# Kernel optimization log

Hardware: AMD Instinct MI355X
Metric: run time of the kernel (lower is better)

Reference implementation:

```python
import jax, jax.numpy as jnp
import numpy as np

NUM_INPUTS = 1024
NUM_HIDDEN = 1024
FORGET_GATE_BIAS = -1.0
EPS = 1e-5


def layer_norm_1d(x, weight, bias):
    # Matches torch LayerNorm1D: std is unbiased (ddof=1), divide by (std + eps)
    mean = jnp.mean(x, axis=1, keepdims=True)
    std = jnp.std(x, axis=1, keepdims=True, ddof=1)
    return (x - mean) / (std + EPS) * weight + bias


def setup_inputs() -> dict:
    key = jax.random.key(0)
    ks = jax.random.split(key, 8)
    B, I, H = 4096, NUM_INPUTS, NUM_HIDDEN
    lim_i = 1.0 / np.sqrt(I)
    lim_h = 1.0 / np.sqrt(H)
    return {
        "inputs": jax.random.normal(ks[0], (B, I), jnp.float32),
        "hx": jax.random.normal(ks[1], (B, H), jnp.float32),
        "cx": jax.random.normal(ks[2], (B, H), jnp.float32),
        "w_i2h": jax.random.uniform(ks[3], (4 * H, I), jnp.float32, -lim_i, lim_i),
        "b_i2h": jax.random.uniform(ks[4], (4 * H,), jnp.float32, -lim_i, lim_i),
        "w_h2h": jax.random.uniform(ks[5], (4 * H, H), jnp.float32, -lim_h, lim_h),
        "b_h2h": jax.random.uniform(ks[6], (4 * H,), jnp.float32, -lim_h, lim_h),
        "ln_i2h_w": jnp.ones((1, 4 * H), jnp.float32),
        "ln_i2h_b": jnp.zeros((1, 4 * H), jnp.float32),
        "ln_h2h_w": jnp.ones((1, 4 * H), jnp.float32),
        "ln_h2h_b": jnp.zeros((1, 4 * H), jnp.float32),
        "ln_h2o_w": jnp.ones((1, H), jnp.float32),
        "ln_h2o_b": jnp.zeros((1, H), jnp.float32),
    }


def reference(inputs, hx, cx, w_i2h, b_i2h, w_h2h, b_h2h,
              ln_i2h_w, ln_i2h_b, ln_h2h_w, ln_h2h_b, ln_h2o_w, ln_h2o_b):
    H = NUM_HIDDEN
    i2h = inputs @ w_i2h.T + b_i2h          # [B, 4H]
    h2h = hx @ w_h2h.T + b_h2h              # [B, 4H]
    x = layer_norm_1d(i2h, ln_i2h_w, ln_i2h_b) + layer_norm_1d(h2h, ln_h2h_w, ln_h2h_b)
    g_i, g_f, g_o, g_c = jnp.split(x, 4, axis=1)
    in_gate = jax.nn.sigmoid(g_i)
    forget_gate = jax.nn.sigmoid(g_f + FORGET_GATE_BIAS)
    out_gate = jax.nn.sigmoid(g_o)
    in_transform = jnp.tanh(g_c)
    cx_new = forget_gate * cx + in_gate * in_transform
    hx_new = out_gate * jnp.tanh(layer_norm_1d(cx_new, ln_h2o_w, ln_h2o_b))
    return hx_new, cx_new
```

## Files before the change

### kernel.cpp

```cpp
#include <hip/hip_runtime.h>
#include <hip/hip_bf16.h>
#include <math.h>

#define NI 1024
#define NH 1024
#define H4 4096
#define FGB (-1.0f)
#define LN_EPS 1e-5f
#define NKT 32

typedef unsigned short u16;
typedef __attribute__((ext_vector_type(8))) short short8;
typedef __attribute__((ext_vector_type(8))) unsigned short ushort8v;
typedef __attribute__((ext_vector_type(16))) float f32x16;

__device__ __forceinline__ float bf2f(u16 u) {
    union { unsigned int i; float f; } v; v.i = ((unsigned int)u) << 16; return v.f;
}
__device__ __forceinline__ u16 f2bf(float f) {
    __hip_bfloat16 h = __float2bfloat16(f);
    return __builtin_bit_cast(u16, h);
}
__device__ __forceinline__ float fast_sigmoid(float x) {
    return 1.0f / (1.0f + __expf(-x));
}
__device__ __forceinline__ float fast_tanh(float x) {
    return 1.0f - 2.0f / (__expf(2.0f * x) + 1.0f);
}

__device__ __forceinline__ void gload16(const u16* g, u16* l) {
    __builtin_amdgcn_global_load_lds(
        (const __attribute__((address_space(1))) void*)g,
        (__attribute__((address_space(3))) void*)l,
        16, 0, 0);
}

__global__ __launch_bounds__(256) void shuffle_cast(
    const float* __restrict__ a, const float* __restrict__ b,
    const float* __restrict__ c, const float* __restrict__ d,
    u16* __restrict__ oa, u16* __restrict__ ob,
    u16* __restrict__ oc, u16* __restrict__ od)
{
    __shared__ u16 sT[32][264];

    const int my = blockIdx.y;
    const float* src = (my == 0) ? a : (my == 1) ? b : (my == 2) ? c : d;
    u16*         dst = (my == 0) ? oa : (my == 1) ? ob : (my == 2) ? oc : od;

    const int mtile = blockIdx.x >> 2;
    const int slab  = blockIdx.x & 3;
    const int t     = threadIdx.x;
    const int w     = t >> 6;
    const int lane  = t & 63;

    const float* s0 = src + (size_t)(mtile * 32) * 1024 + slab * 256 + lane * 4;
#pragma unroll
    for (int i = 0; i < 8; ++i) {
        const int row = i * 4 + w;
        float4 v = *(const float4*)(s0 + (size_t)row * 1024);
        ushort4 pk;
        pk.x = f2bf(v.x); pk.y = f2bf(v.y); pk.z = f2bf(v.z); pk.w = f2bf(v.w);
        *(ushort4*)&sT[row][lane * 4] = pk;
    }
    __syncthreads();

    const int r  = lane & 31;
    const int hi = lane >> 5;
#pragma unroll
    for (int j = 0; j < 2; ++j) {
        const int ktl = w * 2 + j;
        const int kt  = slab * 8 + ktl;
        u16* o = dst + ((size_t)(mtile * 32 + kt)) * 1024 + lane * 8;
#pragma unroll
        for (int kh = 0; kh < 2; ++kh) {
            ushort8v vv = *(const ushort8v*)&sT[r][ktl * 32 + kh * 16 + hi * 8];
            *(ushort8v*)(o + kh * 512) = vv;
        }
    }
}

__global__ __launch_bounds__(512, 2) void gemm_lds(
    const u16* __restrict__ Af0, const u16* __restrict__ Wf0,
    const float* __restrict__ bias0, u16* __restrict__ C0,
    const u16* __restrict__ Af1, const u16* __restrict__ Wf1,
    const float* __restrict__ bias1, u16* __restrict__ C1,
    int N)
{
    const u16*   Af   = blockIdx.z ? Af1 : Af0;
    const u16*   Wf   = blockIdx.z ? Wf1 : Wf0;
    const float* bias = blockIdx.z ? bias1 : bias0;
    u16*         C    = blockIdx.z ? C1 : C0;

    __shared__ __align__(16) u16 sA[4][8][2][512];
    __shared__ __align__(16) u16 sB[4][8][2][512];

    const int tid  = threadIdx.x;
    const int lane = tid & 63;
    const int wave = tid >> 6;
    const int wm   = wave >> 2;
    const int wn   = wave & 3;

    const u16* gA = Af + (size_t)(blockIdx.y * 8 + wave) * 32768 + lane * 8;
    const u16* gB = Wf + (size_t)(blockIdx.x * 8 + wave) * 32768 + lane * 8;

    f32x16 acc[4][2];
#pragma unroll
    for (int i = 0; i < 4; ++i)
#pragma unroll
        for (int j = 0; j < 2; ++j)
#pragma unroll
            for (int r = 0; r < 16; ++r)
                acc[i][j][r] = 0.f;

#define STAGE(kt)                                                            \
    do {                                                                     \
        gload16(gA + (size_t)(kt) * 1024,       &sA[(kt) & 3][wave][0][0]);  \
        gload16(gA + (size_t)(kt) * 1024 + 512, &sA[(kt) & 3][wave][1][0]);  \
        gload16(gB + (size_t)(kt) * 1024,       &sB[(kt) & 3][wave][0][0]);  \
        gload16(gB + (size_t)(kt) * 1024 + 512, &sB[(kt) & 3][wave][1][0]);  \
    } while (0)

    ushort8v a0_0, a1_0, a2_0, a3_0, b0_0, b1_0;
    ushort8v a0_1, a1_1, a2_1, a3_1, b0_1, b1_1;

#define R0(slot)                                                             \
    do {                                                                     \
        a0_0 = *(const ushort8v*)&sA[slot][wm * 4 + 0][0][lane * 8];         \
        a1_0 = *(const ushort8v*)&sA[slot][wm * 4 + 1][0][lane * 8];         \
        b0_0 = *(const ushort8v*)&sB[slot][wn * 2 + 0][0][lane * 8];         \
        b1_0 = *(const ushort8v*)&sB[slot][wn * 2 + 1][0][lane * 8];         \
        a2_0 = *(const ushort8v*)&sA[slot][wm * 4 + 2][0][lane * 8];         \
        a3_0 = *(const ushort8v*)&sA[slot][wm * 4 + 3][0][lane * 8];         \
    } while (0)
#define R1(slot)                                                             \
    do {                                                                     \
        a0_1 = *(const ushort8v*)&sA[slot][wm * 4 + 0][1][lane * 8];         \
        a1_1 = *(const ushort8v*)&sA[slot][wm * 4 + 1][1][lane * 8];         \
        b0_1 = *(const ushort8v*)&sB[slot][wn * 2 + 0][1][lane * 8];         \
        b1_1 = *(const ushort8v*)&sB[slot][wn * 2 + 1][1][lane * 8];         \
        a2_1 = *(const ushort8v*)&sA[slot][wm * 4 + 2][1][lane * 8];         \
        a3_1 = *(const ushort8v*)&sA[slot][wm * 4 + 3][1][lane * 8];         \
    } while (0)

#define M8(aa0, aa1, aa2, aa3, bb0, bb1)                                                             \
    do {                                                                                             \
        __builtin_amdgcn_s_setprio(1);                                                               \
        acc[0][0] = __builtin_amdgcn_mfma_f32_32x32x16_bf16((short8)aa0, (short8)bb0, acc[0][0], 0, 0, 0); \
        acc[1][0] = __builtin_amdgcn_mfma_f32_32x32x16_bf16((short8)aa1, (short8)bb0, acc[1][0], 0, 0, 0); \
        acc[0][1] = __builtin_amdgcn_mfma_f32_32x32x16_bf16((short8)aa0, (short8)bb1, acc[0][1], 0, 0, 0); \
        acc[1][1] = __builtin_amdgcn_mfma_f32_32x32x16_bf16((short8)aa1, (short8)bb1, acc[1][1], 0, 0, 0); \
        acc[2][0] = __builtin_amdgcn_mfma_f32_32x32x16_bf16((short8)aa2, (short8)bb0, acc[2][0], 0, 0, 0); \
        acc[3][0] = __builtin_amdgcn_mfma_f32_32x32x16_bf16((short8)aa3, (short8)bb0, acc[3][0], 0, 0, 0); \
        acc[2][1] = __builtin_amdgcn_mfma_f32_32x32x16_bf16((short8)aa2, (short8)bb1, acc[2][1], 0, 0, 0); \
        acc[3][1] = __builtin_amdgcn_mfma_f32_32x32x16_bf16((short8)aa3, (short8)bb1, acc[3][1], 0, 0, 0); \
        __builtin_amdgcn_s_setprio(0);                                                               \
    } while (0)

#define M8_SET0() M8(a0_0, a1_0, a2_0, a3_0, b0_0, b1_0)
#define M8_SET1() M8(a0_1, a1_1, a2_1, a3_1, b0_1, b1_1)

#define FENCE() asm volatile("" ::: "memory")

    STAGE(0);
    STAGE(1);
    asm volatile("s_waitcnt vmcnt(4)" ::: "memory");
    FENCE();
    __builtin_amdgcn_s_barrier();
    FENCE();
    STAGE(2);
    R0(0);
    R1(0);
    M8_SET0();

#pragma unroll
    for (int kt = 1; kt < NKT; ++kt) {
        const int slot = kt & 3;
        if (kt == NKT - 1) {
            asm volatile("s_waitcnt vmcnt(0)" ::: "memory");
        } else {
            asm volatile("s_waitcnt vmcnt(4)" ::: "memory");
        }
        FENCE();
        __builtin_amdgcn_s_barrier();
        FENCE();
        if (kt + 2 < NKT) STAGE(kt + 2);
        R0(slot);
        M8_SET1();
        R1(slot);
        M8_SET0();
    }
    M8_SET1();

#undef STAGE
#undef R0
#undef R1
#undef M8
#undef M8_SET0
#undef M8_SET1
#undef FENCE

    const int m0  = blockIdx.y * 256;
    const int n0  = blockIdx.x * 256;
    const int l31 = lane & 31;
    float bv[2];
#pragma unroll
    for (int tn = 0; tn < 2; ++tn)
        bv[tn] = bias[n0 + wn * 64 + tn * 32 + l31];

    const int rbase = (lane >> 5) * 4;
#pragma unroll
    for (int tm = 0; tm < 4; ++tm)
#pragma unroll
        for (int reg = 0; reg < 16; ++reg) {
            const int row = m0 + wm * 128 + tm * 32 + (reg & 3) + 8 * (reg >> 2) + rbase;
#pragma unroll
            for (int tn = 0; tn < 2; ++tn) {
                const int col = n0 + wn * 64 + tn * 32 + l31;
                C[(size_t)row * N + col] = f2bf(acc[tm][tn][reg] + bv[tn]);
            }
        }
}

__global__ __launch_bounds__(256) void lstm_pointwise(
    const u16* __restrict__ i2h, const u16* __restrict__ h2h,
    const float* __restrict__ cx,
    const float* __restrict__ lwx, const float* __restrict__ lbx,
    const float* __restrict__ lwy, const float* __restrict__ lby,
    const float* __restrict__ lwc, const float* __restrict__ lbc,
    float* __restrict__ hx_out, float* __restrict__ cx_out)
{
    __shared__ u16 sX[H4];
    __shared__ u16 sY[H4];
    __shared__ float red[16];

    const int row  = blockIdx.x;
    const int tid  = threadIdx.x;
    const int lane = tid & 63;
    const int wid  = tid >> 6;

    const u16* xr = i2h + (size_t)row * H4;
    const u16* yr = h2h + (size_t)row * H4;

    float sx = 0.f, sxx = 0.f, sy = 0.f, syy = 0.f;
#pragma unroll
    for (int s = 0; s < 2; ++s) {
        const int off = s * 2048 + tid * 8;
        ushort8v xv = *(const ushort8v*)(xr + off);
        ushort8v yv = *(const ushort8v*)(yr + off);
        *(ushort8v*)(sX + off) = xv;
        *(ushort8v*)(sY + off) = yv;
#pragma unroll
        for (int e = 0; e < 8; ++e) {
            float x = bf2f(xv[e]), y = bf2f(yv[e]);
            sx += x; sxx += x * x; sy += y; syy += y * y;
        }
    }
#pragma unroll
    for (int m = 32; m; m >>= 1) {
        sx  += __shfl_xor(sx,  m, 64);
        sxx += __shfl_xor(sxx, m, 64);
        sy  += __shfl_xor(sy,  m, 64);
        syy += __shfl_xor(syy, m, 64);
    }
    if (lane == 0) {
        red[wid] = sx; red[4 + wid] = sxx; red[8 + wid] = sy; red[12 + wid] = syy;
    }
    __syncthreads();
    const float tsx  = red[0] + red[1] + red[2] + red[3];
    const float tsxx = red[4] + red[5] + red[6] + red[7];
    const float tsy  = red[8] + red[9] + red[10] + red[11];
    const float tsyy = red[12] + red[13] + red[14] + red[15];
    __syncthreads();

    const float n1  = (float)H4;
    const float mx  = tsx / n1;
    const float ivx = 1.0f / (sqrtf(fmaxf((tsxx - tsx * tsx / n1) / (n1 - 1.f), 0.f)) + LN_EPS);
    const float my  = tsy / n1;
    const float ivy = 1.0f / (sqrtf(fmaxf((tsyy - tsy * tsy / n1) / (n1 - 1.f), 0.f)) + LN_EPS);

    const int j0 = tid * 4;
    float gate[4][4];
#pragma unroll
    for (int g = 0; g < 4; ++g) {
        ushort4 xv = *(const ushort4*)(sX + g * NH + j0);
        ushort4 yv = *(const ushort4*)(sY + g * NH + j0);
        float4 wxv = *(const float4*)(lwx + g * NH + j0);
        float4 bxv = *(const float4*)(lbx + g * NH + j0);
        float4 wyv = *(const float4*)(lwy + g * NH + j0);
        float4 byv = *(const float4*)(lby + g * NH + j0);
        gate[g][0] = (bf2f(xv.x) - mx) * ivx * wxv.x + bxv.x + (bf2f(yv.x) - my) * ivy * wyv.x + byv.x;
        gate[g][1] = (bf2f(xv.y) - mx) * ivx * wxv.y + bxv.y + (bf2f(yv.y) - my) * ivy * wyv.y + byv.y;
        gate[g][2] = (bf2f(xv.z) - mx) * ivx * wxv.z + bxv.z + (bf2f(yv.z) - my) * ivy * wyv.z + byv.z;
        gate[g][3] = (bf2f(xv.w) - mx) * ivx * wxv.w + bxv.w + (bf2f(yv.w) - my) * ivy * wyv.w + byv.w;
    }

    float4 cxv = *(const float4*)(cx + (size_t)row * NH + j0);
    const float cin[4] = {cxv.x, cxv.y, cxv.z, cxv.w};
    float cvl[4], og[4];
    float sc = 0.f, scc = 0.f;
#pragma unroll
    for (int e = 0; e < 4; ++e) {
        float ing = fast_sigmoid(gate[0][e]);
        float fg  = fast_sigmoid(gate[1][e] + FGB);
        og[e]     = fast_sigmoid(gate[2][e]);
        float tr  = fast_tanh(gate[3][e]);
        float c   = fg * cin[e] + ing * tr;
        cvl[e] = c; sc += c; scc += c * c;
    }
    *(float4*)(cx_out + (size_t)row * NH + j0) = make_float4(cvl[0], cvl[1], cvl[2], cvl[3]);

#pragma unroll
    for (int m = 32; m; m >>= 1) {
        sc  += __shfl_xor(sc,  m, 64);
        scc += __shfl_xor(scc, m, 64);
    }
    if (lane == 0) { red[wid] = sc; red[4 + wid] = scc; }
    __syncthreads();
    const float tsc  = red[0] + red[1] + red[2] + red[3];
    const float tscc = red[4] + red[5] + red[6] + red[7];

    const float nc  = (float)NH;
    const float mc  = tsc / nc;
    const float ivc = 1.0f / (sqrtf(fmaxf((tscc - tsc * tsc / nc) / (nc - 1.f), 0.f)) + LN_EPS);

    float4 wcv = *(const float4*)(lwc + j0);
    float4 bcv = *(const float4*)(lbc + j0);
    float h0 = og[0] * fast_tanh((cvl[0] - mc) * ivc * wcv.x + bcv.x);
    float h1 = og[1] * fast_tanh((cvl[1] - mc) * ivc * wcv.y + bcv.y);
    float h2 = og[2] * fast_tanh((cvl[2] - mc) * ivc * wcv.z + bcv.z);
    float h3 = og[3] * fast_tanh((cvl[3] - mc) * ivc * wcv.w + bcv.w);
    *(float4*)(hx_out + (size_t)row * NH + j0) = make_float4(h0, h1, h2, h3);
}

extern "C" void kernel_launch(void* const* d_in, const int* in_sizes, int n_in,
                              void* d_out, int out_size, void* d_ws, size_t ws_size,
                              hipStream_t stream) {
    const float* inputs = (const float*)d_in[0];
    const float* hx     = (const float*)d_in[1];
    const float* cx     = (const float*)d_in[2];
    const float* w_i2h  = (const float*)d_in[3];
    const float* b_i2h  = (const float*)d_in[4];
    const float* w_h2h  = (const float*)d_in[5];
    const float* b_h2h  = (const float*)d_in[6];
    const float* lwx    = (const float*)d_in[7];
    const float* lbx    = (const float*)d_in[8];
    const float* lwy    = (const float*)d_in[9];
    const float* lby    = (const float*)d_in[10];
    const float* lwc    = (const float*)d_in[11];
    const float* lbc    = (const float*)d_in[12];

    const int B = in_sizes[0] / NI;

    u16* a_fr   = (u16*)d_ws;
    u16* hx_fr  = a_fr   + (size_t)B * NI;
    u16* wi_fr  = hx_fr  + (size_t)B * NH;
    u16* wh_fr  = wi_fr  + (size_t)H4 * NI;
    u16* i2h_bf = wh_fr  + (size_t)H4 * NH;
    u16* h2h_bf = i2h_bf + (size_t)B * H4;

    float* hx_out = (float*)d_out;
    float* cx_out = hx_out + (size_t)B * NH;

    shuffle_cast<<<dim3(512, 4), dim3(256), 0, stream>>>(
        inputs, hx, w_i2h, w_h2h, a_fr, hx_fr, wi_fr, wh_fr);

    gemm_lds<<<dim3(H4 / 256, B / 256, 2), dim3(512), 0, stream>>>(
        a_fr, wi_fr, b_i2h, i2h_bf,
        hx_fr, wh_fr, b_h2h, h2h_bf,
        H4);

    lstm_pointwise<<<dim3(B), dim3(256), 0, stream>>>(
        i2h_bf, h2h_bf, cx, lwx, lbx, lwy, lby, lwc, lbc, hx_out, cx_out);
}
```

Baseline: 245.0 us.

## Use 4 waves per GEMM block with 128x128 warp tiles

Measured after the change: 250.7 us. +2.3%, slower.

```diff
diff --git a/kernel.cpp b/kernel.cpp
--- a/kernel.cpp
+++ b/kernel.cpp
@@ -79,7 +79,7 @@
     }
 }
 
-__global__ __launch_bounds__(512, 2) void gemm_lds(
+__global__ __launch_bounds__(256, 1) void gemm_lds(
     const u16* __restrict__ Af0, const u16* __restrict__ Wf0,
     const float* __restrict__ bias0, u16* __restrict__ C0,
     const u16* __restrict__ Af1, const u16* __restrict__ Wf1,
@@ -97,80 +97,90 @@
     const int tid  = threadIdx.x;
     const int lane = tid & 63;
     const int wave = tid >> 6;
-    const int wm   = wave >> 2;
-    const int wn   = wave & 3;
-
-    const u16* gA = Af + (size_t)(blockIdx.y * 8 + wave) * 32768 + lane * 8;
-    const u16* gB = Wf + (size_t)(blockIdx.x * 8 + wave) * 32768 + lane * 8;
-
-    f32x16 acc[4][2];
+    const int wm   = wave >> 1;
+    const int wn   = wave & 1;
+
+    const u16* gA0 = Af + (size_t)(blockIdx.y * 8 + wave * 2 + 0) * 32768 + lane * 8;
+    const u16* gA1 = Af + (size_t)(blockIdx.y * 8 + wave * 2 + 1) * 32768 + lane * 8;
+    const u16* gB0 = Wf + (size_t)(blockIdx.x * 8 + wave * 2 + 0) * 32768 + lane * 8;
+    const u16* gB1 = Wf + (size_t)(blockIdx.x * 8 + wave * 2 + 1) * 32768 + lane * 8;
+
+    f32x16 acc[4][4];
 #pragma unroll
     for (int i = 0; i < 4; ++i)
 #pragma unroll
-        for (int j = 0; j < 2; ++j)
+        for (int j = 0; j < 4; ++j)
 #pragma unroll
             for (int r = 0; r < 16; ++r)
                 acc[i][j][r] = 0.f;
 
-#define STAGE(kt)                                                            \
-    do {                                                                     \
-        gload16(gA + (size_t)(kt) * 1024,       &sA[(kt) & 3][wave][0][0]);  \
-        gload16(gA + (size_t)(kt) * 1024 + 512, &sA[(kt) & 3][wave][1][0]);  \
-        gload16(gB + (size_t)(kt) * 1024,       &sB[(kt) & 3][wave][0][0]);  \
-        gload16(gB + (size_t)(kt) * 1024 + 512, &sB[(kt) & 3][wave][1][0]);  \
+#define STAGE(kt)                                                             \
+    do {                                                                      \
+        gload16(gA0 + (size_t)(kt) * 1024,       &sA[(kt) & 3][wave * 2 + 0][0][0]); \
+        gload16(gA0 + (size_t)(kt) * 1024 + 512, &sA[(kt) & 3][wave * 2 + 0][1][0]); \
+        gload16(gA1 + (size_t)(kt) * 1024,       &sA[(kt) & 3][wave * 2 + 1][0][0]); \
+        gload16(gA1 + (size_t)(kt) * 1024 + 512, &sA[(kt) & 3][wave * 2 + 1][1][0]); \
+        gload16(gB0 + (size_t)(kt) * 1024,       &sB[(kt) & 3][wave * 2 + 0][0][0]); \
+        gload16(gB0 + (size_t)(kt) * 1024 + 512, &sB[(kt) & 3][wave * 2 + 0][1][0]); \
+        gload16(gB1 + (size_t)(kt) * 1024,       &sB[(kt) & 3][wave * 2 + 1][0][0]); \
+        gload16(gB1 + (size_t)(kt) * 1024 + 512, &sB[(kt) & 3][wave * 2 + 1][1][0]); \
     } while (0)
 
-    ushort8v a0_0, a1_0, a2_0, a3_0, b0_0, b1_0;
-    ushort8v a0_1, a1_1, a2_1, a3_1, b0_1, b1_1;
+    ushort8v a0_0, a1_0, a2_0, a3_0, b0_0, b1_0, b2_0, b3_0;
+    ushort8v a0_1, a1_1, a2_1, a3_1, b0_1, b1_1, b2_1, b3_1;
 
 #define R0(slot)                                                             \
     do {                                                                     \
         a0_0 = *(const ushort8v*)&sA[slot][wm * 4 + 0][0][lane * 8];         \
+        b0_0 = *(const ushort8v*)&sB[slot][wn * 4 + 0][0][lane * 8];         \
         a1_0 = *(const ushort8v*)&sA[slot][wm * 4 + 1][0][lane * 8];         \
-        b0_0 = *(const ushort8v*)&sB[slot][wn * 2 + 0][0][lane * 8];         \
-        b1_0 = *(const ushort8v*)&sB[slot][wn * 2 + 1][0][lane * 8];         \
+        b1_0 = *(const ushort8v*)&sB[slot][wn * 4 + 1][0][lane * 8];         \
         a2_0 = *(const ushort8v*)&sA[slot][wm * 4 + 2][0][lane * 8];         \
+        b2_0 = *(const ushort8v*)&sB[slot][wn * 4 + 2][0][lane * 8];         \
         a3_0 = *(const ushort8v*)&sA[slot][wm * 4 + 3][0][lane * 8];         \
+        b3_0 = *(const ushort8v*)&sB[slot][wn * 4 + 3][0][lane * 8];         \
     } while (0)
 #define R1(slot)                                                             \
     do {                                                                     \
         a0_1 = *(const ushort8v*)&sA[slot][wm * 4 + 0][1][lane * 8];         \
+        b0_1 = *(const ushort8v*)&sB[slot][wn * 4 + 0][1][lane * 8];         \
         a1_1 = *(const ushort8v*)&sA[slot][wm * 4 + 1][1][lane * 8];         \
-        b0_1 = *(const ushort8v*)&sB[slot][wn * 2 + 0][1][lane * 8];         \
-        b1_1 = *(const ushort8v*)&sB[slot][wn * 2 + 1][1][lane * 8];         \
+        b1_1 = *(const ushort8v*)&sB[slot][wn * 4 + 1][1][lane * 8];         \
         a2_1 = *(const ushort8v*)&sA[slot][wm * 4 + 2][1][lane * 8];         \
+        b2_1 = *(const ushort8v*)&sB[slot][wn * 4 + 2][1][lane * 8];         \
         a3_1 = *(const ushort8v*)&sA[slot][wm * 4 + 3][1][lane * 8];         \
+        b3_1 = *(const ushort8v*)&sB[slot][wn * 4 + 3][1][lane * 8];         \
     } while (0)
 
-#define M8(aa0, aa1, aa2, aa3, bb0, bb1)                                                             \
-    do {                                                                                             \
-        __builtin_amdgcn_s_setprio(1);                                                               \
-        acc[0][0] = __builtin_amdgcn_mfma_f32_32x32x16_bf16((short8)aa0, (short8)bb0, acc[0][0], 0, 0, 0); \
-        acc[1][0] = __builtin_amdgcn_mfma_f32_32x32x16_bf16((short8)aa1, (short8)bb0, acc[1][0], 0, 0, 0); \
-        acc[0][1] = __builtin_amdgcn_mfma_f32_32x32x16_bf16((short8)aa0, (short8)bb1, acc[0][1], 0, 0, 0); \
-        acc[1][1] = __builtin_amdgcn_mfma_f32_32x32x16_bf16((short8)aa1, (short8)bb1, acc[1][1], 0, 0, 0); \
-        acc[2][0] = __builtin_amdgcn_mfma_f32_32x32x16_bf16((short8)aa2, (short8)bb0, acc[2][0], 0, 0, 0); \
-        acc[3][0] = __builtin_amdgcn_mfma_f32_32x32x16_bf16((short8)aa3, (short8)bb0, acc[3][0], 0, 0, 0); \
-        acc[2][1] = __builtin_amdgcn_mfma_f32_32x32x16_bf16((short8)aa2, (short8)bb1, acc[2][1], 0, 0, 0); \
-        acc[3][1] = __builtin_amdgcn_mfma_f32_32x32x16_bf16((short8)aa3, (short8)bb1, acc[3][1], 0, 0, 0); \
-        __builtin_amdgcn_s_setprio(0);                                                               \
+#define MM(i, j, aa, bb) \
+    acc[i][j] = __builtin_amdgcn_mfma_f32_32x32x16_bf16((short8)aa, (short8)bb, acc[i][j], 0, 0, 0)
+
+#define M16(s)                                                               \
+    do {                                                                     \
+        __builtin_amdgcn_s_setprio(1);                                       \
+        MM(0, 0, a0_##s, b0_##s); MM(1, 0, a1_##s, b0_##s);                  \
+        MM(0, 1, a0_##s, b1_##s); MM(1, 1, a1_##s, b1_##s);                  \
+        MM(2, 0, a2_##s, b0_##s); MM(3, 0, a3_##s, b0_##s);                  \
+        MM(2, 1, a2_##s, b1_##s); MM(3, 1, a3_##s, b1_##s);                  \
+        MM(0, 2, a0_##s, b2_##s); MM(1, 2, a1_##s, b2_##s);                  \
+        MM(0, 3, a0_##s, b3_##s); MM(1, 3, a1_##s, b3_##s);                  \
+        MM(2, 2, a2_##s, b2_##s); MM(3, 2, a3_##s, b2_##s);                  \
+        MM(2, 3, a2_##s, b3_##s); MM(3, 3, a3_##s, b3_##s);                  \
+        __builtin_amdgcn_s_setprio(0);                                       \
     } while (0)
-
-#define M8_SET0() M8(a0_0, a1_0, a2_0, a3_0, b0_0, b1_0)
-#define M8_SET1() M8(a0_1, a1_1, a2_1, a3_1, b0_1, b1_1)
 
 #define FENCE() asm volatile("" ::: "memory")
 
     STAGE(0);
     STAGE(1);
-    asm volatile("s_waitcnt vmcnt(4)" ::: "memory");
+    asm volatile("s_waitcnt vmcnt(8)" ::: "memory");
     FENCE();
     __builtin_amdgcn_s_barrier();
     FENCE();
     STAGE(2);
     R0(0);
     R1(0);
-    M8_SET0();
+    M16(0);
 
 #pragma unroll
     for (int kt = 1; kt < NKT; ++kt) {
@@ -178,34 +188,33 @@
         if (kt == NKT - 1) {
             asm volatile("s_waitcnt vmcnt(0)" ::: "memory");
         } else {
-            asm volatile("s_waitcnt vmcnt(4)" ::: "memory");
+            asm volatile("s_waitcnt vmcnt(8)" ::: "memory");
         }
         FENCE();
         __builtin_amdgcn_s_barrier();
         FENCE();
         if (kt + 2 < NKT) STAGE(kt + 2);
         R0(slot);
-        M8_SET1();
+        M16(1);
         R1(slot);
-        M8_SET0();
-    }
-    M8_SET1();
+        M16(0);
+    }
+    M16(1);
 
 #undef STAGE
 #undef R0
 #undef R1
-#undef M8
-#undef M8_SET0
-#undef M8_SET1
+#undef MM
+#undef M16
 #undef FENCE
 
     const int m0  = blockIdx.y * 256;
     const int n0  = blockIdx.x * 256;
     const int l31 = lane & 31;
-    float bv[2];
-#pragma unroll
-    for (int tn = 0; tn < 2; ++tn)
-        bv[tn] = bias[n0 + wn * 64 + tn * 32 + l31];
+    float bv[4];
+#pragma unroll
+    for (int tn = 0; tn < 4; ++tn)
+        bv[tn] = bias[n0 + wn * 128 + tn * 32 + l31];
 
     const int rbase = (lane >> 5) * 4;
 #pragma unroll
@@ -214,8 +223,8 @@
         for (int reg = 0; reg < 16; ++reg) {
             const int row = m0 + wm * 128 + tm * 32 + (reg & 3) + 8 * (reg >> 2) + rbase;
 #pragma unroll
-            for (int tn = 0; tn < 2; ++tn) {
-                const int col = n0 + wn * 64 + tn * 32 + l31;
+            for (int tn = 0; tn < 4; ++tn) {
+                const int col = n0 + wn * 128 + tn * 32 + l31;
                 C[(size_t)row * N + col] = f2bf(acc[tm][tn][reg] + bv[tn]);
             }
         }
@@ -364,7 +373,7 @@
     shuffle_cast<<<dim3(512, 4), dim3(256), 0, stream>>>(
         inputs, hx, w_i2h, w_h2h, a_fr, hx_fr, wi_fr, wh_fr);
 
-    gemm_lds<<<dim3(H4 / 256, B / 256, 2), dim3(512), 0, stream>>>(
+    gemm_lds<<<dim3(H4 / 256, B / 256, 2), dim3(256), 0, stream>>>(
         a_fr, wi_fr, b_i2h, i2h_bf,
         hx_fr, wh_fr, b_h2h, h2h_bf,
         H4);
```

## Stagger LDS reads and MFMA order across wave pairs; keep pointwise rows in registers

Applied to the files above, without the earlier changes.

Result: faster. 237.6 us (-3.0%).

```diff
diff --git a/kernel.cpp b/kernel.cpp
--- a/kernel.cpp
+++ b/kernel.cpp
@@ -126,8 +126,8 @@
 #define R0(slot)                                                             \
     do {                                                                     \
         a0_0 = *(const ushort8v*)&sA[slot][wm * 4 + 0][0][lane * 8];         \
+        b0_0 = *(const ushort8v*)&sB[slot][wn * 2 + 0][0][lane * 8];         \
         a1_0 = *(const ushort8v*)&sA[slot][wm * 4 + 1][0][lane * 8];         \
-        b0_0 = *(const ushort8v*)&sB[slot][wn * 2 + 0][0][lane * 8];         \
         b1_0 = *(const ushort8v*)&sB[slot][wn * 2 + 1][0][lane * 8];         \
         a2_0 = *(const ushort8v*)&sA[slot][wm * 4 + 2][0][lane * 8];         \
         a3_0 = *(const ushort8v*)&sA[slot][wm * 4 + 3][0][lane * 8];         \
@@ -135,31 +135,39 @@
 #define R1(slot)                                                             \
     do {                                                                     \
         a0_1 = *(const ushort8v*)&sA[slot][wm * 4 + 0][1][lane * 8];         \
+        b0_1 = *(const ushort8v*)&sB[slot][wn * 2 + 0][1][lane * 8];         \
         a1_1 = *(const ushort8v*)&sA[slot][wm * 4 + 1][1][lane * 8];         \
-        b0_1 = *(const ushort8v*)&sB[slot][wn * 2 + 0][1][lane * 8];         \
         b1_1 = *(const ushort8v*)&sB[slot][wn * 2 + 1][1][lane * 8];         \
         a2_1 = *(const ushort8v*)&sA[slot][wm * 4 + 2][1][lane * 8];         \
         a3_1 = *(const ushort8v*)&sA[slot][wm * 4 + 3][1][lane * 8];         \
     } while (0)
 
-#define M8(aa0, aa1, aa2, aa3, bb0, bb1)                                                             \
-    do {                                                                                             \
-        __builtin_amdgcn_s_setprio(1);                                                               \
-        acc[0][0] = __builtin_amdgcn_mfma_f32_32x32x16_bf16((short8)aa0, (short8)bb0, acc[0][0], 0, 0, 0); \
-        acc[1][0] = __builtin_amdgcn_mfma_f32_32x32x16_bf16((short8)aa1, (short8)bb0, acc[1][0], 0, 0, 0); \
-        acc[0][1] = __builtin_amdgcn_mfma_f32_32x32x16_bf16((short8)aa0, (short8)bb1, acc[0][1], 0, 0, 0); \
-        acc[1][1] = __builtin_amdgcn_mfma_f32_32x32x16_bf16((short8)aa1, (short8)bb1, acc[1][1], 0, 0, 0); \
-        acc[2][0] = __builtin_amdgcn_mfma_f32_32x32x16_bf16((short8)aa2, (short8)bb0, acc[2][0], 0, 0, 0); \
-        acc[3][0] = __builtin_amdgcn_mfma_f32_32x32x16_bf16((short8)aa3, (short8)bb0, acc[3][0], 0, 0, 0); \
-        acc[2][1] = __builtin_amdgcn_mfma_f32_32x32x16_bf16((short8)aa2, (short8)bb1, acc[2][1], 0, 0, 0); \
-        acc[3][1] = __builtin_amdgcn_mfma_f32_32x32x16_bf16((short8)aa3, (short8)bb1, acc[3][1], 0, 0, 0); \
-        __builtin_amdgcn_s_setprio(0);                                                               \
-    } while (0)
-
-#define M8_SET0() M8(a0_0, a1_0, a2_0, a3_0, b0_0, b1_0)
-#define M8_SET1() M8(a0_1, a1_1, a2_1, a3_1, b0_1, b1_1)
+#define MM(i, j, aa, bb) \
+    acc[i][j] = __builtin_amdgcn_mfma_f32_32x32x16_bf16((short8)aa, (short8)bb, acc[i][j], 0, 0, 0)
+
+#define M8(s)                                                                \
+    do {                                                                     \
+        __builtin_amdgcn_s_setprio(1);                                       \
+        MM(0, 0, a0_##s, b0_##s); MM(1, 0, a1_##s, b0_##s);                  \
+        MM(0, 1, a0_##s, b1_##s); MM(1, 1, a1_##s, b1_##s);                  \
+        MM(2, 0, a2_##s, b0_##s); MM(3, 0, a3_##s, b0_##s);                  \
+        MM(2, 1, a2_##s, b1_##s); MM(3, 1, a3_##s, b1_##s);                  \
+        __builtin_amdgcn_s_setprio(0);                                       \
+    } while (0)
 
 #define FENCE() asm volatile("" ::: "memory")
+#define WIN_TOP(kt)                                                          \
+    do {                                                                     \
+        if ((kt) == NKT - 1) {                                               \
+            asm volatile("s_waitcnt vmcnt(0)" ::: "memory");                 \
+        } else {                                                             \
+            asm volatile("s_waitcnt vmcnt(4)" ::: "memory");                 \
+        }                                                                    \
+        FENCE();                                                             \
+        __builtin_amdgcn_s_barrier();                                        \
+        FENCE();                                                             \
+        if ((kt) + 2 < NKT) STAGE((kt) + 2);                                 \
+    } while (0)
 
     STAGE(0);
     STAGE(1);
@@ -170,33 +178,38 @@
     STAGE(2);
     R0(0);
     R1(0);
-    M8_SET0();
-
-#pragma unroll
-    for (int kt = 1; kt < NKT; ++kt) {
-        const int slot = kt & 3;
-        if (kt == NKT - 1) {
-            asm volatile("s_waitcnt vmcnt(0)" ::: "memory");
-        } else {
-            asm volatile("s_waitcnt vmcnt(4)" ::: "memory");
-        }
-        FENCE();
-        __builtin_amdgcn_s_barrier();
-        FENCE();
-        if (kt + 2 < NKT) STAGE(kt + 2);
-        R0(slot);
-        M8_SET1();
-        R1(slot);
-        M8_SET0();
-    }
-    M8_SET1();
+    M8(0);
+
+    if ((wave & 1) == 0) {
+#pragma unroll
+        for (int kt = 1; kt < NKT; ++kt) {
+            const int slot = kt & 3;
+            WIN_TOP(kt);
+            R0(slot);
+            M8(1);
+            R1(slot);
+            M8(0);
+        }
+    } else {
+#pragma unroll
+        for (int kt = 1; kt < NKT; ++kt) {
+            const int slot = kt & 3;
+            WIN_TOP(kt);
+            M8(1);
+            __builtin_amdgcn_sched_barrier(0);
+            R0(slot);
+            R1(slot);
+            M8(0);
+        }
+    }
+    M8(1);
 
 #undef STAGE
 #undef R0
 #undef R1
+#undef MM
 #undef M8
-#undef M8_SET0
-#undef M8_SET1
+#undef WIN_TOP
 #undef FENCE
 
     const int m0  = blockIdx.y * 256;
@@ -229,30 +242,31 @@
     const float* __restrict__ lwc, const float* __restrict__ lbc,
     float* __restrict__ hx_out, float* __restrict__ cx_out)
 {
-    __shared__ u16 sX[H4];
-    __shared__ u16 sY[H4];
     __shared__ float red[16];
 
     const int row  = blockIdx.x;
     const int tid  = threadIdx.x;
     const int lane = tid & 63;
     const int wid  = tid >> 6;
+    const int j0   = tid * 4;
 
     const u16* xr = i2h + (size_t)row * H4;
     const u16* yr = h2h + (size_t)row * H4;
 
+    float xf[4][4], yf[4][4];
     float sx = 0.f, sxx = 0.f, sy = 0.f, syy = 0.f;
 #pragma unroll
-    for (int s = 0; s < 2; ++s) {
-        const int off = s * 2048 + tid * 8;
-        ushort8v xv = *(const ushort8v*)(xr + off);
-        ushort8v yv = *(const ushort8v*)(yr + off);
-        *(ushort8v*)(sX + off) = xv;
-        *(ushort8v*)(sY + off) = yv;
-#pragma unroll
-        for (int e = 0; e < 8; ++e) {
-            float x = bf2f(xv[e]), y = bf2f(yv[e]);
-            sx += x; sxx += x * x; sy += y; syy += y * y;
+    for (int g = 0; g < 4; ++g) {
+        ushort4 xv = *(const ushort4*)(xr + g * NH + j0);
+        ushort4 yv = *(const ushort4*)(yr + g * NH + j0);
+        xf[g][0] = bf2f(xv.x); xf[g][1] = bf2f(xv.y);
+        xf[g][2] = bf2f(xv.z); xf[g][3] = bf2f(xv.w);
+        yf[g][0] = bf2f(yv.x); yf[g][1] = bf2f(yv.y);
+        yf[g][2] = bf2f(yv.z); yf[g][3] = bf2f(yv.w);
+#pragma unroll
+        for (int e = 0; e < 4; ++e) {
+            sx += xf[g][e]; sxx += xf[g][e] * xf[g][e];
+            sy += yf[g][e]; syy += yf[g][e] * yf[g][e];
         }
     }
 #pragma unroll
@@ -270,7 +284,6 @@
     const float tsxx = red[4] + red[5] + red[6] + red[7];
     const float tsy  = red[8] + red[9] + red[10] + red[11];
     const float tsyy = red[12] + red[13] + red[14] + red[15];
-    __syncthreads();
 
     const float n1  = (float)H4;
     const float mx  = tsx / n1;
@@ -278,20 +291,17 @@
     const float my  = tsy / n1;
     const float ivy = 1.0f / (sqrtf(fmaxf((tsyy - tsy * tsy / n1) / (n1 - 1.f), 0.f)) + LN_EPS);
 
-    const int j0 = tid * 4;
     float gate[4][4];
 #pragma unroll
     for (int g = 0; g < 4; ++g) {
-        ushort4 xv = *(const ushort4*)(sX + g * NH + j0);
-        ushort4 yv = *(const ushort4*)(sY + g * NH + j0);
         float4 wxv = *(const float4*)(lwx + g * NH + j0);
         float4 bxv = *(const float4*)(lbx + g * NH + j0);
         float4 wyv = *(const float4*)(lwy + g * NH + j0);
         float4 byv = *(const float4*)(lby + g * NH + j0);
-        gate[g][0] = (bf2f(xv.x) - mx) * ivx * wxv.x + bxv.x + (bf2f(yv.x) - my) * ivy * wyv.x + byv.x;
-        gate[g][1] = (bf2f(xv.y) - mx) * ivx * wxv.y + bxv.y + (bf2f(yv.y) - my) * ivy * wyv.y + byv.y;
-        gate[g][2] = (bf2f(xv.z) - mx) * ivx * wxv.z + bxv.z + (bf2f(yv.z) - my) * ivy * wyv.z + byv.z;
-        gate[g][3] = (bf2f(xv.w) - mx) * ivx * wxv.w + bxv.w + (bf2f(yv.w) - my) * ivy * wyv.w + byv.w;
+        gate[g][0] = (xf[g][0] - mx) * ivx * wxv.x + bxv.x + (yf[g][0] - my) * ivy * wyv.x + byv.x;
+        gate[g][1] = (xf[g][1] - mx) * ivx * wxv.y + bxv.y + (yf[g][1] - my) * ivy * wyv.y + byv.y;
+        gate[g][2] = (xf[g][2] - mx) * ivx * wxv.z + bxv.z + (yf[g][2] - my) * ivy * wyv.z + byv.z;
+        gate[g][3] = (xf[g][3] - mx) * ivx * wxv.w + bxv.w + (yf[g][3] - my) * ivy * wyv.w + byv.w;
     }
 
     float4 cxv = *(const float4*)(cx + (size_t)row * NH + j0);
@@ -314,6 +324,7 @@
         sc  += __shfl_xor(sc,  m, 64);
         scc += __shfl_xor(scc, m, 64);
     }
+    __syncthreads();
     if (lane == 0) { red[wid] = sc; red[4 + wid] = scc; }
     __syncthreads();
     const float tsc  = red[0] + red[1] + red[2] + red[3];
```
